# Performance work log

Measured on AMD Instinct MI355X. Metric: run time of the kernel, lower is better.

## Reference

```python
import jax, jax.numpy as jnp
import numpy as np

N_NODES = 10000
N_EDGES = 160000
IN_DIM = 256
HEADS = 8
C0 = 32   # per-head out channels, layer 0 (256 // 8)
C1 = 32   # per-head out channels, layer 1 (= output_dim)
RANK = 8
LORA_SCALE = 32.0 / 8      # alpha / rank
ATT_RANK = 4               # rank // 2
ATT_SCALE = 32.0 / 4       # alpha / (rank // 2)
NEG_SLOPE = 0.2


def _gat_layer(x, src, dst, W, A, B, att_s, att_d, As, Bs, Ad, Bd, concat):
    """One LoRAGATConv layer (eval mode, dropout=0)."""
    N = x.shape[0]
    H, C = att_s.shape
    # LoRA-adapted projection: base + B(A x) * scaling -> [N, H, C]
    xp = (x @ W.T + ((x @ A.T) @ B.T) * LORA_SCALE).reshape(N, H, C)

    def att_score(base, Aa, Ba):
        # per-head base dot product + LoRA(out_channels -> 1) path -> [N, H]
        return jnp.einsum('nhc,hc->nh', xp, base) + ((xp @ Aa.T) @ Ba.T)[..., 0] * ATT_SCALE

    s_src = att_score(att_s, As, Bs)  # applied to x_i (destination), per original code
    s_dst = att_score(att_d, Ad, Bd)  # applied to x_j (source), per original code

    alpha = s_src[dst] + s_dst[src]              # [E, H]
    alpha = jax.nn.leaky_relu(alpha, NEG_SLOPE)
    # segment softmax over destination nodes (every node has a self-loop)
    m = jax.ops.segment_max(alpha, dst, num_segments=N)
    e = jnp.exp(alpha - m[dst])
    den = jax.ops.segment_sum(e, dst, num_segments=N)
    a = e / den[dst]                             # [E, H]

    msg = xp[src] * a[:, :, None]                # [E, H, C]
    out = jax.ops.segment_sum(msg, dst, num_segments=N)  # [N, H, C]
    return out.reshape(N, H * C) if concat else out.mean(axis=1)


def _forward(x, edge_index,
             W0, A0, B0, att_src0, att_dst0, Asrc0, Bsrc0, Adst0, Bdst0,
             W1, A1, B1, att_src1, att_dst1, Asrc1, Bsrc1, Adst1, Bdst1):
    N = x.shape[0]
    loops = jnp.arange(N, dtype=edge_index.dtype)
    ei = jnp.concatenate([edge_index, jnp.stack([loops, loops])], axis=1)
    src, dst = ei[0], ei[1]
    h = _gat_layer(x, src, dst, W0, A0, B0, att_src0, att_dst0, Asrc0, Bsrc0, Adst0, Bdst0, concat=True)
    h = jax.nn.elu(h)
    out = _gat_layer(h, src, dst, W1, A1, B1, att_src1, att_dst1, Asrc1, Bsrc1, Adst1, Bdst1, concat=False)
    return out


def setup_inputs() -> dict:
    key = jax.random.key(0)
    ks = jax.random.split(key, 24)
    s = 0.05
    inp = {
        'x': jax.random.normal(ks[0], (N_NODES, IN_DIM), dtype=jnp.float32),
        'edge_index': jax.random.randint(ks[1], (2, N_EDGES), 0, N_NODES, dtype=jnp.int64),
    }
    # layer 0: in 256 -> heads*C0 = 256
    inp['W0'] = jax.random.normal(ks[2], (HEADS * C0, IN_DIM), dtype=jnp.float32) * s
    inp['A0'] = jax.random.normal(ks[3], (RANK, IN_DIM), dtype=jnp.float32) * s
    inp['B0'] = jax.random.normal(ks[4], (HEADS * C0, RANK), dtype=jnp.float32) * s
    inp['att_src0'] = jax.random.normal(ks[5], (HEADS, C0), dtype=jnp.float32) * s
    inp['att_dst0'] = jax.random.normal(ks[6], (HEADS, C0), dtype=jnp.float32) * s
    inp['Asrc0'] = jax.random.normal(ks[7], (ATT_RANK, C0), dtype=jnp.float32) * s
    inp['Bsrc0'] = jax.random.normal(ks[8], (1, ATT_RANK), dtype=jnp.float32) * s
    inp['Adst0'] = jax.random.normal(ks[9], (ATT_RANK, C0), dtype=jnp.float32) * s
    inp['Bdst0'] = jax.random.normal(ks[10], (1, ATT_RANK), dtype=jnp.float32) * s
    # layer 1: in heads*C0 = 256 -> heads*C1 = 256 (head-averaged -> 32)
    D1 = HEADS * C0
    inp['W1'] = jax.random.normal(ks[11], (HEADS * C1, D1), dtype=jnp.float32) * s
    inp['A1'] = jax.random.normal(ks[12], (RANK, D1), dtype=jnp.float32) * s
    inp['B1'] = jax.random.normal(ks[13], (HEADS * C1, RANK), dtype=jnp.float32) * s
    inp['att_src1'] = jax.random.normal(ks[14], (HEADS, C1), dtype=jnp.float32) * s
    inp['att_dst1'] = jax.random.normal(ks[15], (HEADS, C1), dtype=jnp.float32) * s
    inp['Asrc1'] = jax.random.normal(ks[16], (ATT_RANK, C1), dtype=jnp.float32) * s
    inp['Bsrc1'] = jax.random.normal(ks[17], (1, ATT_RANK), dtype=jnp.float32) * s
    inp['Adst1'] = jax.random.normal(ks[18], (ATT_RANK, C1), dtype=jnp.float32) * s
    inp['Bdst1'] = jax.random.normal(ks[19], (1, ATT_RANK), dtype=jnp.float32) * s
    return inp


def reference(x, edge_index,
              W0, A0, B0, att_src0, att_dst0, Asrc0, Bsrc0, Adst0, Bdst0,
              W1, A1, B1, att_src1, att_dst1, Asrc1, Bsrc1, Adst1, Bdst1):
    return _forward(x, edge_index,
                    W0, A0, B0, att_src0, att_dst0, Asrc0, Bsrc0, Adst0, Bdst0,
                    W1, A1, B1, att_src1, att_dst1, Asrc1, Bsrc1, Adst1, Bdst1)
```

## Files before the change

kernel.cpp:

```cpp
#include <hip/hip_runtime.h>

#define LORA_SCALE 4.0f
#define ATT_SCALE 8.0f
#define NEG_SLOPE 0.2f
#define ELLW 64

typedef __attribute__((ext_vector_type(8))) short bf16x8;
typedef __attribute__((ext_vector_type(4))) float f32x4;
typedef unsigned short ushort_t;
typedef unsigned int uint_t;

__device__ inline ushort_t f2bf(float f) {
    uint_t u = __float_as_uint(f);
    u += 0x7fff + ((u >> 16) & 1);
    return (ushort_t)(u >> 16);
}
__device__ inline float bf2f(ushort_t h) {
    return __uint_as_float(((uint_t)h) << 16);
}
__device__ inline void split_bf(float f, ushort_t& h, ushort_t& l) {
    h = f2bf(f);
    l = f2bf(f - bf2f(h));
}

__global__ void prep_all(const float* __restrict__ W0, const float* __restrict__ A0,
                         const float* __restrict__ B0,
                         const float* __restrict__ att_s0, const float* __restrict__ att_d0,
                         const float* __restrict__ As0, const float* __restrict__ Bs0,
                         const float* __restrict__ Ad0, const float* __restrict__ Bd0,
                         const float* __restrict__ W1, const float* __restrict__ A1,
                         const float* __restrict__ B1,
                         const float* __restrict__ att_s1, const float* __restrict__ att_d1,
                         const float* __restrict__ As1, const float* __restrict__ Bs1,
                         const float* __restrict__ Ad1, const float* __restrict__ Bd1,
                         ushort_t* __restrict__ whi0, ushort_t* __restrict__ wlo0,
                         ushort_t* __restrict__ whi1, ushort_t* __restrict__ wlo1,
                         float* __restrict__ effS0, float* __restrict__ effD0,
                         float* __restrict__ effS1, float* __restrict__ effD1,
                         const float* __restrict__ x, ushort_t* __restrict__ xhi,
                         ushort_t* __restrict__ xlo,
                         const int* __restrict__ ei, int E_real, int E_total,
                         int* __restrict__ cnt, int* __restrict__ ell, int N)
{
    int b = blockIdx.x;
    int t = threadIdx.x;
    if (b < 512) {
        int layer = b >> 8;
        int i = (b & 255) * 256 + t;
        const float* W = layer ? W1 : W0;
        const float* A = layer ? A1 : A0;
        const float* B = layer ? B1 : B0;
        int r = i >> 8, c = i & 255;
        float acc = W[i];
        #pragma unroll
        for (int k = 0; k < 8; k++) acc += LORA_SCALE * B[r * 8 + k] * A[k * 256 + c];
        ushort_t h, l;
        split_bf(acc, h, l);
        if (layer) { whi1[i] = h; wlo1[i] = l; }
        else       { whi0[i] = h; wlo0[i] = l; }
        if (i < 256) {
            int c2 = i & 31;
            const float* as_ = layer ? att_s1 : att_s0;
            const float* ad_ = layer ? att_d1 : att_d0;
            const float* As = layer ? As1 : As0;
            const float* Bs = layer ? Bs1 : Bs0;
            const float* Ad = layer ? Ad1 : Ad0;
            const float* Bd = layer ? Bd1 : Bd0;
            float es = as_[i], ed = ad_[i];
            #pragma unroll
            for (int k = 0; k < 4; k++) {
                es += ATT_SCALE * Bs[k] * As[k * 32 + c2];
                ed += ATT_SCALE * Bd[k] * Ad[k * 32 + c2];
            }
            if (layer) { effS1[i] = es; effD1[i] = ed; }
            else       { effS0[i] = es; effD0[i] = ed; }
        }
        return;
    }
    int cb = b - 512;
    int convB = (N * 64 + 255) / 256;
    if (cb < convB) {
        int i = cb * 256 + t;
        if (i >= N * 64) return;
        float4 v = *(const float4*)(x + i * 4);
        ushort4 hs, ls;
        split_bf(v.x, hs.x, ls.x);
        split_bf(v.y, hs.y, ls.y);
        split_bf(v.z, hs.z, ls.z);
        split_bf(v.w, hs.w, ls.w);
        *(ushort4*)(xhi + i * 4) = hs;
        *(ushort4*)(xlo + i * 4) = ls;
        return;
    }
    int e = (cb - convB) * 256 + t;
    if (e >= E_total) return;
    int s, d;
    if (e < E_real) { s = ei[e]; d = ei[E_real + e]; }
    else            { s = d = e - E_real; }
    int pos = atomicAdd(&cnt[d], 1);
    if (pos < ELLW) ell[d * ELLW + pos] = s;
}

__global__ __launch_bounds__(64) void gemm_fused(
    const ushort_t* __restrict__ Ahi, const ushort_t* __restrict__ Alo,
    const ushort_t* __restrict__ Bhi, const ushort_t* __restrict__ Blo,
    const float* __restrict__ effS, const float* __restrict__ effD,
    ushort_t* __restrict__ Cb, float* __restrict__ ssrc, float* __restrict__ sdst, int M)
{
    const int K = 256;
    int lane = threadIdx.x;
    int quad = lane >> 4;
    int l16 = lane & 15;
    int m0 = blockIdx.y * 16;
    int n0 = blockIdx.x * 64;
    int mr = m0 + l16; if (mr >= M) mr = M - 1;

    const ushort_t* ah = Ahi + mr * K + quad * 8;
    const ushort_t* al = Alo + mr * K + quad * 8;
    const ushort_t* bh = Bhi + (n0 + l16) * K + quad * 8;
    const ushort_t* bl = Blo + (n0 + l16) * K + quad * 8;

    f32x4 acc[4] = {};
    #pragma unroll
    for (int k0 = 0; k0 < K; k0 += 32) {
        bf16x8 a_hi = *(const bf16x8*)(ah + k0);
        bf16x8 a_lo = *(const bf16x8*)(al + k0);
        #pragma unroll
        for (int t = 0; t < 4; t++) {
            bf16x8 b_hi = *(const bf16x8*)(bh + t * 16 * K + k0);
            bf16x8 b_lo = *(const bf16x8*)(bl + t * 16 * K + k0);
            acc[t] = __builtin_amdgcn_mfma_f32_16x16x32_bf16(a_hi, b_hi, acc[t], 0, 0, 0);
            acc[t] = __builtin_amdgcn_mfma_f32_16x16x32_bf16(a_hi, b_lo, acc[t], 0, 0, 0);
            acc[t] = __builtin_amdgcn_mfma_f32_16x16x32_bf16(a_lo, b_hi, acc[t], 0, 0, 0);
        }
    }

    #pragma unroll
    for (int t = 0; t < 4; t++) {
        #pragma unroll
        for (int r = 0; r < 4; r++) {
            int m = m0 + quad * 4 + r;
            if (m < M) Cb[m * 256 + n0 + t * 16 + l16] = f2bf(acc[t][r]);
        }
    }

    int h0 = n0 >> 5;
    float vs[2][4], vd[2][4];
    #pragma unroll
    for (int g = 0; g < 2; g++) {
        float e0s = effS[n0 + 32 * g + l16];
        float e1s = effS[n0 + 32 * g + 16 + l16];
        float e0d = effD[n0 + 32 * g + l16];
        float e1d = effD[n0 + 32 * g + 16 + l16];
        #pragma unroll
        for (int r = 0; r < 4; r++) {
            vs[g][r] = acc[2 * g][r] * e0s + acc[2 * g + 1][r] * e1s;
            vd[g][r] = acc[2 * g][r] * e0d + acc[2 * g + 1][r] * e1d;
        }
    }
    #pragma unroll
    for (int m = 1; m <= 8; m <<= 1) {
        #pragma unroll
        for (int g = 0; g < 2; g++)
            #pragma unroll
            for (int r = 0; r < 4; r++) {
                vs[g][r] += __shfl_xor(vs[g][r], m);
                vd[g][r] += __shfl_xor(vd[g][r], m);
            }
    }
    if (l16 == 0) {
        #pragma unroll
        for (int g = 0; g < 2; g++)
            #pragma unroll
            for (int r = 0; r < 4; r++) {
                int m = m0 + quad * 4 + r;
                if (m < M) {
                    ssrc[m * 8 + h0 + g] = vs[g][r];
                    sdst[m * 8 + h0 + g] = vd[g][r];
                }
            }
    }
}

__global__ __launch_bounds__(256) void ell_agg(const int* __restrict__ cnt,
                                               const int* __restrict__ ell,
                                               const ushort_t* __restrict__ xpb,
                                               const float* __restrict__ ssrc,
                                               const float* __restrict__ sdst,
                                               float* __restrict__ out,
                                               ushort_t* __restrict__ ohi,
                                               ushort_t* __restrict__ olo,
                                               int N, int mode)
{
    __shared__ int sidx[4][ELLW];
    int gid = blockIdx.x * blockDim.x + threadIdx.x;
    int d = gid >> 6;
    if (d >= N) return;
    int w = threadIdx.x >> 6;
    int lane = threadIdx.x & 63;
    int h = lane >> 3;
    float ssrc_h = ssrc[d * 8 + h];
    int end = cnt[d]; if (end > ELLW) end = ELLW;
    const int* row = ell + d * ELLW;
    sidx[w][lane] = row[lane < end ? lane : 0];

    float den = 0.f, ax = 0.f, ay = 0.f, az = 0.f, aw = 0.f;
    for (int i = 0; i < end; i += 8) {
        int idx[8];
        #pragma unroll
        for (int j = 0; j < 8; j++) {
            int ii = i + j;
            idx[j] = sidx[w][ii < end ? ii : 0];
        }
        float t[8];
        #pragma unroll
        for (int j = 0; j < 8; j++) t[j] = sdst[idx[j] * 8 + h];
        ushort4 v[8];
        #pragma unroll
        for (int j = 0; j < 8; j++) v[j] = *(const ushort4*)(xpb + idx[j] * 256 + lane * 4);
        float w8[8];
        #pragma unroll
        for (int j = 0; j < 8; j++) {
            float al = ssrc_h + t[j];
            al = al > 0.f ? al : NEG_SLOPE * al;
            w8[j] = (i + j < end) ? __expf(al) : 0.f;
        }
        #pragma unroll
        for (int j = 0; j < 8; j++) {
            den += w8[j];
            ax += bf2f(v[j].x) * w8[j];
            ay += bf2f(v[j].y) * w8[j];
            az += bf2f(v[j].z) * w8[j];
            aw += bf2f(v[j].w) * w8[j];
        }
    }
    float inv = 1.f / den;
    ax *= inv; ay *= inv; az *= inv; aw *= inv;

    if (mode == 2) {
        #pragma unroll
        for (int m = 8; m <= 32; m <<= 1) {
            ax += __shfl_xor(ax, m);
            ay += __shfl_xor(ay, m);
            az += __shfl_xor(az, m);
            aw += __shfl_xor(aw, m);
        }
        if (lane < 8) {
            float4 r = { ax * 0.125f, ay * 0.125f, az * 0.125f, aw * 0.125f };
            *(float4*)(out + d * 32 + lane * 4) = r;
        }
        return;
    }
    ax = ax > 0.f ? ax : (__expf(ax) - 1.f);
    ay = ay > 0.f ? ay : (__expf(ay) - 1.f);
    az = az > 0.f ? az : (__expf(az) - 1.f);
    aw = aw > 0.f ? aw : (__expf(aw) - 1.f);
    ushort4 hs, ls;
    split_bf(ax, hs.x, ls.x);
    split_bf(ay, hs.y, ls.y);
    split_bf(az, hs.z, ls.z);
    split_bf(aw, hs.w, ls.w);
    *(ushort4*)(ohi + d * 256 + lane * 4) = hs;
    *(ushort4*)(olo + d * 256 + lane * 4) = ls;
}

extern "C" void kernel_launch(void* const* d_in, const int* in_sizes, int n_in,
                              void* d_out, int out_size, void* d_ws, size_t ws_size,
                              hipStream_t stream)
{
    const float* x  = (const float*)d_in[0];
    const int*   ei = (const int*)d_in[1];
    const float* W0 = (const float*)d_in[2];
    const float* A0 = (const float*)d_in[3];
    const float* B0 = (const float*)d_in[4];
    const float* att_s0 = (const float*)d_in[5];
    const float* att_d0 = (const float*)d_in[6];
    const float* As0 = (const float*)d_in[7];
    const float* Bs0 = (const float*)d_in[8];
    const float* Ad0 = (const float*)d_in[9];
    const float* Bd0 = (const float*)d_in[10];
    const float* W1 = (const float*)d_in[11];
    const float* A1 = (const float*)d_in[12];
    const float* B1 = (const float*)d_in[13];
    const float* att_s1 = (const float*)d_in[14];
    const float* att_d1 = (const float*)d_in[15];
    const float* As1 = (const float*)d_in[16];
    const float* Bs1 = (const float*)d_in[17];
    const float* Ad1 = (const float*)d_in[18];
    const float* Bd1 = (const float*)d_in[19];

    const int N = in_sizes[0] / 256;
    const int E_real = in_sizes[1] / 2;
    const int E_total = E_real + N;

    ushort_t* whi0 = (ushort_t*)d_ws;
    ushort_t* wlo0 = whi0 + 65536;
    ushort_t* whi1 = wlo0 + 65536;
    ushort_t* wlo1 = whi1 + 65536;
    ushort_t* xhi  = wlo1 + 65536;
    ushort_t* xlo  = xhi + 2560000;
    ushort_t* hbhi = xlo + 2560000;
    ushort_t* hblo = hbhi + 2560000;
    ushort_t* xpb  = hblo + 2560000;
    float* effS0 = (float*)(xpb + 2560000);
    float* effD0 = effS0 + 256;
    float* effS1 = effD0 + 256;
    float* effD1 = effS1 + 256;
    float* ssrc  = effD1 + 256;
    float* sdst  = ssrc + 80000;
    int* cnt = (int*)(sdst + 80000);
    int* ell = cnt + 10016;

    hipMemsetAsync(cnt, 0, (size_t)N * sizeof(int), stream);
    int convB = (N * 64 + 255) / 256;
    int fillB = (E_total + 255) / 256;
    prep_all<<<512 + convB + fillB, 256, 0, stream>>>(
        W0, A0, B0, att_s0, att_d0, As0, Bs0, Ad0, Bd0,
        W1, A1, B1, att_s1, att_d1, As1, Bs1, Ad1, Bd1,
        whi0, wlo0, whi1, wlo1, effS0, effD0, effS1, effD1,
        x, xhi, xlo, ei, E_real, E_total, cnt, ell, N);

    dim3 gg(4, (N + 15) / 16);
    int aggBlocks = (N * 64 + 255) / 256;

    gemm_fused<<<gg, 64, 0, stream>>>(xhi, xlo, whi0, wlo0, effS0, effD0, xpb, ssrc, sdst, N);
    ell_agg<<<aggBlocks, 256, 0, stream>>>(cnt, ell, xpb, ssrc, sdst,
                                           nullptr, hbhi, hblo, N, 1);

    gemm_fused<<<gg, 64, 0, stream>>>(hbhi, hblo, whi1, wlo1, effS1, effD1, xpb, ssrc, sdst, N);
    ell_agg<<<aggBlocks, 256, 0, stream>>>(cnt, ell, xpb, ssrc, sdst,
                                           (float*)d_out, nullptr, nullptr, N, 2);
}
```

Before: 193.1 us.

## Stage weight tile in shared memory and share across four waves per block

The GEMM block grows from one wave to four. The 64x256 hi/lo weight slice is loaded once into LDS in an MFMA-friendly swizzled layout, and each wave computes its own 16-row M tile from it. This cuts redundant global/L2 reads of B, which every 16-row block previously fetched separately. The cost is 64KB of LDS per block, which limits occupancy, plus a block-level sync before compute.

```diff
diff --git a/kernel.cpp b/kernel.cpp
--- a/kernel.cpp
+++ b/kernel.cpp
@@ -101,34 +101,53 @@
     if (pos < ELLW) ell[d * ELLW + pos] = s;
 }
 
-__global__ __launch_bounds__(64) void gemm_fused(
+__global__ __launch_bounds__(256) void gemm_fused(
     const ushort_t* __restrict__ Ahi, const ushort_t* __restrict__ Alo,
     const ushort_t* __restrict__ Bhi, const ushort_t* __restrict__ Blo,
     const float* __restrict__ effS, const float* __restrict__ effD,
     ushort_t* __restrict__ Cb, float* __restrict__ ssrc, float* __restrict__ sdst, int M)
 {
+    __shared__ ushort_t sBh[16384];
+    __shared__ ushort_t sBl[16384];
     const int K = 256;
-    int lane = threadIdx.x;
+    int tid = threadIdx.x;
+    int n0 = blockIdx.x * 64;
+
+    const ushort_t* srcH = Bhi + (size_t)n0 * K;
+    const ushort_t* srcL = Blo + (size_t)n0 * K;
+    #pragma unroll
+    for (int c = 0; c < 8; c++) {
+        int g  = c * 256 + tid;
+        int rr = g >> 5;
+        int ch = g & 31;
+        int kblk = ch >> 2, quad = ch & 3;
+        int tt = rr >> 4, l16r = rr & 15;
+        int dst = (((tt * 8 + kblk) * 4 + quad) * 16 + l16r) * 8;
+        *(bf16x8*)&sBh[dst] = *(const bf16x8*)(srcH + rr * K + ch * 8);
+        *(bf16x8*)&sBl[dst] = *(const bf16x8*)(srcL + rr * K + ch * 8);
+    }
+    __syncthreads();
+
+    int w = tid >> 6;
+    int lane = tid & 63;
     int quad = lane >> 4;
     int l16 = lane & 15;
-    int m0 = blockIdx.y * 16;
-    int n0 = blockIdx.x * 64;
+    int m0 = blockIdx.y * 64 + w * 16;
     int mr = m0 + l16; if (mr >= M) mr = M - 1;
 
     const ushort_t* ah = Ahi + mr * K + quad * 8;
     const ushort_t* al = Alo + mr * K + quad * 8;
-    const ushort_t* bh = Bhi + (n0 + l16) * K + quad * 8;
-    const ushort_t* bl = Blo + (n0 + l16) * K + quad * 8;
 
     f32x4 acc[4] = {};
     #pragma unroll
-    for (int k0 = 0; k0 < K; k0 += 32) {
-        bf16x8 a_hi = *(const bf16x8*)(ah + k0);
-        bf16x8 a_lo = *(const bf16x8*)(al + k0);
+    for (int kb = 0; kb < 8; kb++) {
+        bf16x8 a_hi = *(const bf16x8*)(ah + kb * 32);
+        bf16x8 a_lo = *(const bf16x8*)(al + kb * 32);
         #pragma unroll
         for (int t = 0; t < 4; t++) {
-            bf16x8 b_hi = *(const bf16x8*)(bh + t * 16 * K + k0);
-            bf16x8 b_lo = *(const bf16x8*)(bl + t * 16 * K + k0);
+            int off = (((t * 8 + kb) * 4 + quad) * 16 + l16) * 8;
+            bf16x8 b_hi = *(const bf16x8*)&sBh[off];
+            bf16x8 b_lo = *(const bf16x8*)&sBl[off];
             acc[t] = __builtin_amdgcn_mfma_f32_16x16x32_bf16(a_hi, b_hi, acc[t], 0, 0, 0);
             acc[t] = __builtin_amdgcn_mfma_f32_16x16x32_bf16(a_hi, b_lo, acc[t], 0, 0, 0);
             acc[t] = __builtin_amdgcn_mfma_f32_16x16x32_bf16(a_lo, b_hi, acc[t], 0, 0, 0);
@@ -320,14 +339,14 @@
         whi0, wlo0, whi1, wlo1, effS0, effD0, effS1, effD1,
         x, xhi, xlo, ei, E_real, E_total, cnt, ell, N);
 
-    dim3 gg(4, (N + 15) / 16);
+    dim3 gg(4, (N + 63) / 64);
     int aggBlocks = (N * 64 + 255) / 256;
 
-    gemm_fused<<<gg, 64, 0, stream>>>(xhi, xlo, whi0, wlo0, effS0, effD0, xpb, ssrc, sdst, N);
+    gemm_fused<<<gg, 256, 0, stream>>>(xhi, xlo, whi0, wlo0, effS0, effD0, xpb, ssrc, sdst, N);
     ell_agg<<<aggBlocks, 256, 0, stream>>>(cnt, ell, xpb, ssrc, sdst,
                                            nullptr, hbhi, hblo, N, 1);
 
-    gemm_fused<<<gg, 64, 0, stream>>>(hbhi, hblo, whi1, wlo1, effS1, effD1, xpb, ssrc, sdst, N);
+    gemm_fused<<<gg, 256, 0, stream>>>(hbhi, hblo, whi1, wlo1, effS1, effD1, xpb, ssrc, sdst, N);
     ell_agg<<<aggBlocks, 256, 0, stream>>>(cnt, ell, xpb, ssrc, sdst,
                                            (float*)d_out, nullptr, nullptr, N, 2);
 }
```

After: 178.4 us. 7.6% less time.
